# Performance work log

Measured on AMD Instinct MI355X. Metric: run time of the kernel, lower is better.

## Reference

```python
import jax, jax.numpy as jnp
import numpy as np

ALPHA = 0.4  # LeakyReLU negative slope used by the GAT


def _gat_head(h, W, a):
    # h: [N, F], W: [F, Fp], a: [2*Fp]; adjacency is all-ones so no masking
    Wh = h @ W                                   # [N, Fp]
    Fp = W.shape[1]
    e = jax.nn.leaky_relu(Wh @ a[:Fp][:, None] + (Wh @ a[Fp:])[None, :], ALPHA)
    att = jax.nn.softmax(e, axis=-1)             # [N, N]
    return att @ Wh                              # [N, Fp]


def _gat(h, W_heads, a_heads, W_gout, a_gout):
    # multi-head GAT: concat elu(head outputs), then single output attention layer
    heads = jax.vmap(_gat_head, in_axes=(None, 0, 0))(h, W_heads, a_heads)  # [H, N, Fp]
    x = jax.nn.elu(heads).transpose(1, 0, 2).reshape(h.shape[0], -1)        # [N, H*Fp]
    return jax.nn.elu(_gat_head(x, W_gout, a_gout))                          # [N, Cg]


def setup_inputs() -> dict:
    key = jax.random.key(0)
    ks = jax.random.split(key, 20)
    bs, R, S = 4, 512, 54
    h, w = 100, 152
    fc_dim, convs_dim4 = 1024, 512
    Cg, H, So = 256, 4, 128
    Fp = Cg // H
    sc = lambda k, shp, s=0.05: jax.random.normal(k, shp, dtype=jnp.float32) * s
    return {
        'region_f': jax.random.normal(ks[0], (bs * R, fc_dim), dtype=jnp.float32),
        'stuff_f': jax.random.normal(ks[1], (bs, convs_dim4, h, w), dtype=jnp.float32),
        'semseg_score': jax.random.normal(ks[2], (bs, S, h, w), dtype=jnp.float32),
        'W_rin': sc(ks[3], (fc_dim, Cg)), 'b_rin': jnp.zeros((Cg,), jnp.float32),
        'W_sin': sc(ks[4], (convs_dim4, Cg)), 'b_sin': jnp.zeros((Cg,), jnp.float32),
        'W_heads': sc(ks[5], (H, Cg, Fp), 0.1), 'a_heads': sc(ks[6], (H, 2 * Fp), 0.1),
        'W_gout': sc(ks[7], (H * Fp, Cg), 0.1), 'a_gout': sc(ks[8], (2 * Cg,), 0.1),
        'W_rout': sc(ks[9], (Cg, Cg)), 'b_rout': jnp.zeros((Cg,), jnp.float32),
        'W_sout': sc(ks[10], (Cg, So)), 'b_sout': jnp.zeros((So,), jnp.float32),
        'W_seg': sc(ks[11], (convs_dim4 + So, S)), 'b_seg': jnp.zeros((S,), jnp.float32),
    }


def reference(region_f, stuff_f, semseg_score,
              W_rin, b_rin, W_sin, b_sin,
              W_heads, a_heads, W_gout, a_gout,
              W_rout, b_rout, W_sout, b_sout,
              W_seg, b_seg):
    bs, Cd, h, w = stuff_f.shape
    S = semseg_score.shape[1]
    R = region_f.shape[0] // bs
    Cg = W_rin.shape[1]

    # node construction
    region_nodes = region_f @ W_rin + b_rin                           # [bs*R, Cg]
    score_flat = semseg_score.reshape(bs, S, h * w)
    class_center = jnp.einsum('bsn,bcn->bsc',
                              jax.nn.softmax(score_flat, axis=-1),
                              stuff_f.reshape(bs, Cd, h * w))          # [bs, S, Cd]
    class_nodes = class_center @ W_sin + b_sin                         # [bs, S, Cg]

    # per-image dense GAT over region + stuff nodes (batched via vmap)
    nodes = jnp.concatenate([region_nodes.reshape(bs, R, Cg), class_nodes], axis=1)
    graph_nodes = jax.vmap(lambda x: _gat(x, W_heads, a_heads, W_gout, a_gout))(nodes)
    new_region, new_class = graph_nodes[:, :R], graph_nodes[:, R:]

    # new box features: concat of original region features and projected graph features
    new_region_f = jnp.concatenate(
        [region_f, new_region.reshape(bs * R, Cg) @ W_rout + b_rout], axis=-1)

    # new stuff features: scatter class nodes back to pixels via class softmax
    new_class_nodes = new_class @ W_sout + b_sout                      # [bs, S, So]
    attn = jax.nn.softmax(score_flat, axis=1)                          # softmax over classes
    new_stuff = jnp.einsum('bsn,bso->bon', attn, new_class_nodes)      # [bs, So, h*w]
    new_stuff = new_stuff.reshape(bs, -1, h, w)

    # 1x1 conv seg head + x4 bilinear upsample (align_corners=False)
    seg_in = jnp.concatenate([stuff_f, new_stuff], axis=1)
    seg = jnp.einsum('bchw,co->bohw', seg_in, W_seg) + b_seg[None, :, None, None]
    segments = jax.image.resize(seg, (bs, S, 4 * h, 4 * w), method='bilinear')
    return new_region_f, segments
```

## Files before the change

kernel.cpp:

```cpp
#include <hip/hip_runtime.h>

#define HW 15200
#define SSD 54
#define NBATCH 4
#define NNODE 566
#define NPAD 576
#define CGD 256
#define CDD 512
#define NSPLIT 25
#define KSPAN 608

typedef __attribute__((ext_vector_type(4))) float f32x4;
typedef __attribute__((ext_vector_type(8))) short bf16x8;
typedef unsigned short ushort_t;

#define BT_RIN   0
#define BT_SIN   262144
#define BT_HEADS 393216
#define BT_GOUT  458752
#define BT_ROUT  524288
#define BT_SOUT  589824
#define BT_SEG2  622592
#define BT_TOTAL 630784

static constexpr long OFF_P     = 0;
static constexpr long OFF_CC    = OFF_P     + (long)NBATCH*SSD*HW;
static constexpr long OFF_NODES = OFF_CC    + (long)NBATCH*SSD*CDD;
static constexpr long OFF_WH    = OFF_NODES + (long)NBATCH*NNODE*CGD;
static constexpr long OFF_S1    = OFF_WH    + (long)16*NNODE*64;
static constexpr long OFF_S2    = OFF_S1    + 16*NPAD;
static constexpr long OFF_X     = OFF_S2    + 16*NPAD;
static constexpr long OFF_WH2   = OFF_X     + (long)NBATCH*NNODE*CGD;
static constexpr long OFF_S1B   = OFF_WH2   + (long)NBATCH*NNODE*CGD;
static constexpr long OFF_S2B   = OFF_S1B   + NBATCH*NPAD;
static constexpr long OFF_G     = OFF_S2B   + NBATCH*NPAD;
static constexpr long OFF_NCN   = OFF_G     + (long)NBATCH*NNODE*CGD;
static constexpr long OFF_SUMS  = OFF_NCN   + (long)NBATCH*SSD*128;
static constexpr long OFF_BT    = OFF_SUMS  + 256;
static constexpr long OFF_ASEG  = OFF_BT    + (BT_TOTAL/2 + 8);
static constexpr long OFF_SEG   = OFF_ASEG  + (long)NBATCH*64*576/2;
static constexpr long OFF_RFB   = OFF_SEG   + (long)NBATCH*SSD*HW;
static constexpr long OFF_WCOMB = OFF_RFB   + 1048576;
static constexpr long OFF_B2    = OFF_WCOMB + 8192;
static constexpr long OFF_ATTNB = OFF_B2    + 64;

__device__ inline float lrelu04(float x){ return x >= 0.f ? x : 0.4f*x; }
__device__ inline float eluf(float x){ return x > 0.f ? x : __expf(x) - 1.f; }
__device__ inline ushort_t f2bf(float f){
    unsigned u = __float_as_uint(f);
    return (ushort_t)((u + 0x7FFFu + ((u >> 16) & 1u)) >> 16);
}
__device__ inline float bf2f(ushort_t u){ return __uint_as_float((unsigned)u << 16); }
__device__ inline bf16x8 pack8(float4 lo, float4 hi){
    union { bf16x8 v; ushort_t u[8]; } p;
    p.u[0]=f2bf(lo.x); p.u[1]=f2bf(lo.y); p.u[2]=f2bf(lo.z); p.u[3]=f2bf(lo.w);
    p.u[4]=f2bf(hi.x); p.u[5]=f2bf(hi.y); p.u[6]=f2bf(hi.z); p.u[7]=f2bf(hi.w);
    return p.v;
}

__global__ __launch_bounds__(512)
void prep_softmax(const float* __restrict__ score, ushort_t* __restrict__ pb,
                  float* __restrict__ sums, ushort_t* __restrict__ attnb,
                  const float* __restrict__ rf, float* __restrict__ out_region,
                  ushort_t* __restrict__ rfb,
                  const float* __restrict__ W_seg, ushort_t* __restrict__ asegb,
                  const float* __restrict__ W_rin, const float* __restrict__ W_sin,
                  const float* __restrict__ W_heads, const float* __restrict__ W_gout,
                  const float* __restrict__ W_rout, const float* __restrict__ W_sout,
                  const float* __restrict__ b_sout,
                  ushort_t* __restrict__ bt, ushort_t* __restrict__ wcomb,
                  float* __restrict__ bias2, float* __restrict__ s1s2b_zero)
{
    int blk = blockIdx.x;
    int t = threadIdx.x;
    if (blk < 256) {
        int b = blk >> 6, s = blk & 63;
        ushort_t* prow = pb + ((long)b*64 + s)*HW;
        if (s >= SSD) {
            for (int i = t; i < HW; i += 512) prow[i] = 0;
            if (t == 0) sums[b*64 + s] = 1.f;
            return;
        }
        const float* row = score + ((long)b*SSD + s)*HW;
        __shared__ float red[8];
        float s_ = 0.f;
        for (int i = t; i < HW; i += 512) {
            float e = __expf(row[i]);
            s_ += e;
            prow[i] = f2bf(e);
        }
        #pragma unroll
        for (int off = 32; off >= 1; off >>= 1) s_ += __shfl_down(s_, off);
        if ((t & 63) == 0) red[t >> 6] = s_;
        __syncthreads();
        if (t == 0) {
            float tot = 0.f;
            #pragma unroll
            for (int u = 0; u < 8; ++u) tot += red[u];
            sums[b*64 + s] = tot;
        }
        return;
    }
    if (blk < 375) {
        long i = (long)(blk - 256)*512 + t;
        if (i >= (long)NBATCH*HW) return;
        int b = (int)(i / HW), n = (int)(i % HW);
        const float* sp = score + (long)b*SSD*HW + n;
        float v[SSD];
        float m = -1e30f;
        #pragma unroll
        for (int s = 0; s < SSD; ++s) { v[s] = sp[(long)s*HW]; m = fmaxf(m, v[s]); }
        float sum = 0.f;
        #pragma unroll
        for (int s = 0; s < SSD; ++s) { v[s] = __expf(v[s] - m); sum += v[s]; }
        float inv = 1.f / sum;
        ushort_t* ap = attnb + (long)b*64*HW + n;
        #pragma unroll
        for (int s = 0; s < SSD; ++s) ap[(long)s*HW] = f2bf(v[s] * inv);
        #pragma unroll
        for (int s = SSD; s < 64; ++s) ap[(long)s*HW] = 0;
        return;
    }
    long gid = (long)(blk - 375) * 512 + t;
    if (gid < 524288) {
        long row = gid / 256, col = gid % 256;
        float4 v = reinterpret_cast<const float4*>(rf)[gid];
        reinterpret_cast<float4*>(out_region)[row*320 + col] = v;
        union { ushort_t u[4]; uint2 q; } pk;
        pk.u[0]=f2bf(v.x); pk.u[1]=f2bf(v.y); pk.u[2]=f2bf(v.z); pk.u[3]=f2bf(v.w);
        reinterpret_cast<uint2*>(rfb)[gid] = pk.q;
        return;
    }
    gid -= 524288;
    if (gid < 131072) {
        int b = (int)(gid >> 15);
        int r = (int)(gid & 32767);
        int o = r >> 9, k = r & 511;
        asegb[(long)b*36864 + (long)o*576 + k] = f2bf(o < SSD ? W_seg[k*SSD + o] : 0.f);
        return;
    }
    gid -= 131072;
    if (gid < BT_TOTAL) {
        int i = (int)gid;
        float v;
        if (i < BT_SIN)        { int j=i;            int n=j>>10, k=j&1023; v = W_rin[k*256+n]; }
        else if (i < BT_HEADS) { int j=i-BT_SIN;     int n=j>>9,  k=j&511;  v = W_sin[k*256+n]; }
        else if (i < BT_GOUT)  { int j=i-BT_HEADS;   int h=j>>14, r=j&16383; int f=r>>8, k=r&255;
                                 v = W_heads[(h*256+k)*64+f]; }
        else if (i < BT_ROUT)  { int j=i-BT_GOUT;    int n=j>>8,  k=j&255;  v = W_gout[k*256+n]; }
        else if (i < BT_SOUT)  { int j=i-BT_ROUT;    int n=j>>8,  k=j&255;  v = W_rout[k*256+n]; }
        else if (i < BT_SEG2)  { int j=i-BT_SOUT;    int n=j>>8,  k=j&255;  v = W_sout[k*128+n]; }
        else                   { int j=i-BT_SEG2;    int o=j>>7,  k=j&127;
                                 v = (o < SSD) ? W_seg[(512+k)*SSD + o] : 0.f; }
        bt[i] = f2bf(v);
        return;
    }
    gid -= BT_TOTAL;
    if (gid < 16384) {
        int od = (int)(gid >> 8), k = (int)(gid & 255);
        float v = 0.f;
        if (od < SSD)
            for (int o = 0; o < 128; ++o)
                v += W_sout[k*128 + o] * W_seg[(512+o)*SSD + od];
        wcomb[(long)od*256 + k] = f2bf(v);
        return;
    }
    gid -= 16384;
    if (gid < 64) {
        int od = (int)gid;
        float v = 0.f;
        if (od < SSD)
            for (int o = 0; o < 128; ++o)
                v += b_sout[o] * W_seg[(512+o)*SSD + od];
        bias2[od] = v;
        return;
    }
    gid -= 64;
    if (gid < 2L*NBATCH*NPAD)
        s1s2b_zero[gid] = 0.f;
}

__global__ __launch_bounds__(256)
void cc_mfma_v3(const ushort_t* __restrict__ pb, const float* __restrict__ stuff,
                ushort_t* __restrict__ sbout, float* __restrict__ part)
{
    int bid = blockIdx.x;
    int g = (bid >> 6) * 8 + (bid & 7);
    if (g >= NSPLIT*NBATCH) return;
    int nt = (bid >> 3) & 7;
    int ks = g >> 2, b = g & 3;

    int w = threadIdx.x >> 6, l = threadIdx.x & 63;
    int lr = l & 15, lk = l >> 4;
    int n0 = nt*64 + w*16;
    const ushort_t* Prow = pb + ((long)b*64 + lr)*HW;
    const float*    Srow = stuff + ((long)b*CDD + n0 + lr)*HW;
    ushort_t*       Sout = sbout + ((long)b*CDD + n0 + lr)*HW;
    f32x4 acc[4] = {};
    int kbeg = ks * KSPAN;
    for (int k0 = kbeg; k0 < kbeg + KSPAN; k0 += 32) {
        int kk = k0 + lk*8;
        float4 lo = *(const float4*)&Srow[kk];
        float4 hi = *(const float4*)&Srow[kk + 4];
        bf16x8 bfv = pack8(lo, hi);
        *(bf16x8*)&Sout[kk] = bfv;
        #pragma unroll
        for (int mi = 0; mi < 4; ++mi) {
            bf16x8 af = *(const bf16x8*)&Prow[(long)mi*16*HW + kk];
            acc[mi] = __builtin_amdgcn_mfma_f32_16x16x32_bf16(af, bfv, acc[mi], 0, 0, 0);
        }
    }
    int c = n0 + lr;
    #pragma unroll
    for (int mi = 0; mi < 4; ++mi)
        #pragma unroll
        for (int r = 0; r < 4; ++r) {
            int m = mi*16 + lk*4 + r;
            part[(((long)b*NSPLIT + ks)*64 + m)*CDD + c] = acc[mi][r];
        }
}

__global__ __launch_bounds__(256)
void cc_reduce_kernel(const float* __restrict__ part, const float* __restrict__ sums,
                      float* __restrict__ cc)
{
    long i = (long)blockIdx.x * 256 + threadIdx.x;
    const long TOT = (long)NBATCH * SSD * CDD;
    if (i >= TOT) return;
    int b = (int)(i / (SSD * CDD));
    int rem = (int)(i % (SSD * CDD));
    int s = rem / CDD, c = rem % CDD;
    float acc = 0.f;
    for (int ks = 0; ks < NSPLIT; ++ks)
        acc += part[(((long)b*NSPLIT + ks)*64 + s)*CDD + c];
    cc[i] = acc * (1.f / sums[b*64 + s]);
}

template<bool AF32, int OUTMODE>
__device__ __forceinline__
void mm_body(int bx, int by, int bz,
             const void* __restrict__ Ap, const ushort_t* __restrict__ Bt,
             void* __restrict__ Cp, const float* __restrict__ bias,
             int M, int N, int K, int lda, int ldc,
             long sA, int zdivA, long sB, int zmodB, long sC)
{
    int z = bz;
    int w = threadIdx.x >> 6, l = threadIdx.x & 63;
    int lr = l & 15, lk = l >> 4;
    int m0 = bx * 64 + w * 16;
    int n0 = by * 64;
    const ushort_t* bt = Bt + (long)(z % zmodB) * sB;
    int mload = min(m0 + lr, M - 1);
    const float*    Af = (const float*)Ap    + (long)(z / zdivA) * sA + (long)mload * lda;
    const ushort_t* Ab = (const ushort_t*)Ap + (long)(z / zdivA) * sA + (long)mload * lda;
    f32x4 acc[4] = {};

    #pragma unroll 2
    for (int k0 = 0; k0 < K; k0 += 32) {
        int kk = k0 + lk * 8;
        bf16x8 af;
        if (AF32) {
            float4 lo = *(const float4*)&Af[kk];
            float4 hi = *(const float4*)&Af[kk + 4];
            af = pack8(lo, hi);
        } else {
            af = *(const bf16x8*)&Ab[kk];
        }
        #pragma unroll
        for (int j = 0; j < 4; ++j) {
            bf16x8 bf = *(const bf16x8*)&bt[(long)(n0 + j*16 + lr) * K + kk];
            acc[j] = __builtin_amdgcn_mfma_f32_16x16x32_bf16(af, bf, acc[j], 0, 0, 0);
        }
    }

    #pragma unroll
    for (int j = 0; j < 4; ++j) {
        int n = n0 + j*16 + lr;
        float bb = bias ? bias[n] : 0.f;
        #pragma unroll
        for (int r = 0; r < 4; ++r) {
            int m = m0 + lk*4 + r;
            if (OUTMODE == 2) {
                float v = acc[j][r] + bb;
                ((ushort_t*)Cp)[(long)z * sC + (long)n * ldc + m] =
                    (m < M) ? f2bf(v) : (ushort_t)0;
            } else {
                if (m >= M) continue;
                float v = acc[j][r] + bb;
                if (OUTMODE == 0)
                    ((float*)Cp)[(long)z * sC + (long)m * ldc + n] = v;
                else
                    ((ushort_t*)Cp)[(long)z * sC + (long)m * ldc + n] = f2bf(v);
            }
        }
    }
}

__global__ __launch_bounds__(256)
void nodes_both(const ushort_t* __restrict__ rfb, const ushort_t* __restrict__ btRin,
                const float* __restrict__ cc, const ushort_t* __restrict__ btSin,
                ushort_t* __restrict__ nodes,
                const float* __restrict__ b_rin, const float* __restrict__ b_sin)
{
    if (blockIdx.x < 8)
        mm_body<false, 1>(blockIdx.x, blockIdx.y, blockIdx.z,
                          rfb, btRin, nodes, b_rin,
                          512, 256, 1024, 1024, 256, 512L*1024, 1, 0, 1, (long)NNODE*CGD);
    else
        mm_body<true, 1>(0, blockIdx.y, blockIdx.z,
                         cc, btSin, nodes + 512L*CGD, b_sin,
                         SSD, 256, 512, 512, 256, (long)SSD*CDD, 1, 0, 1, (long)NNODE*CGD);
}

__global__ __launch_bounds__(256)
void wht_heads(const ushort_t* __restrict__ nodes, const ushort_t* __restrict__ btHeads,
               ushort_t* __restrict__ wht, const float* __restrict__ a_heads,
               float* __restrict__ s1, float* __restrict__ s2)
{
    int bx = blockIdx.x, z = blockIdx.y;
    int w = threadIdx.x >> 6, l = threadIdx.x & 63;
    int lr = l & 15, lk = l >> 4;
    int m0 = bx*64 + w*16;
    const ushort_t* bt = btHeads + (long)(z & 3) * (64L*256);
    int mload = min(m0 + lr, NNODE - 1);
    const ushort_t* Ab = nodes + (long)(z >> 2)*((long)NNODE*CGD) + (long)mload*CGD;
    f32x4 acc[4] = {};

    #pragma unroll 2
    for (int k0 = 0; k0 < 256; k0 += 32) {
        int kk = k0 + lk*8;
        bf16x8 af = *(const bf16x8*)&Ab[kk];
        #pragma unroll
        for (int j = 0; j < 4; ++j) {
            bf16x8 bf = *(const bf16x8*)&bt[(long)(j*16 + lr)*256 + kk];
            acc[j] = __builtin_amdgcn_mfma_f32_16x16x32_bf16(af, bf, acc[j], 0, 0, 0);
        }
    }

    const float* av = a_heads + (long)(z & 3)*128;
    ushort_t* Wout = wht + (long)z*(64L*NPAD);
    float p1[4] = {0.f,0.f,0.f,0.f}, p2[4] = {0.f,0.f,0.f,0.f};
    #pragma unroll
    for (int j = 0; j < 4; ++j) {
        int f = j*16 + lr;
        float c1 = av[f], c2 = av[64 + f];
        #pragma unroll
        for (int r = 0; r < 4; ++r) {
            int m = m0 + lk*4 + r;
            float v = acc[j][r];
            Wout[(long)f*NPAD + m] = (m < NNODE) ? f2bf(v) : (ushort_t)0;
            if (m < NNODE) { p1[r] += v*c1; p2[r] += v*c2; }
        }
    }
    #pragma unroll
    for (int r = 0; r < 4; ++r)
        #pragma unroll
        for (int off = 1; off < 16; off <<= 1) {
            p1[r] += __shfl_xor(p1[r], off);
            p2[r] += __shfl_xor(p2[r], off);
        }
    if (lr == 0) {
        #pragma unroll
        for (int r = 0; r < 4; ++r) {
            int m = m0 + lk*4 + r;
            if (m < NNODE) {
                s1[(long)z*NPAD + m] = p1[r];
                s2[(long)z*NPAD + m] = p2[r];
            }
        }
    }
}

__global__ __launch_bounds__(256)
void wht2_gout(const ushort_t* __restrict__ xbuf, const ushort_t* __restrict__ btGout,
               ushort_t* __restrict__ wht2, const float* __restrict__ a_gout,
               float* __restrict__ s1b, float* __restrict__ s2b)
{
    int bx = blockIdx.x, by = blockIdx.y, z = blockIdx.z;
    int w = threadIdx.x >> 6, l = threadIdx.x & 63;
    int lr = l & 15, lk = l >> 4;
    int m0 = bx*64 + w*16;
    int n0 = by*64;
    int mload = min(m0 + lr, NNODE - 1);
    const ushort_t* Ab = xbuf + (long)z*((long)NNODE*CGD) + (long)mload*CGD;
    f32x4 acc[4] = {};

    #pragma unroll 2
    for (int k0 = 0; k0 < 256; k0 += 32) {
        int kk = k0 + lk*8;
        bf16x8 af = *(const bf16x8*)&Ab[kk];
        #pragma unroll
        for (int j = 0; j < 4; ++j) {
            bf16x8 bf = *(const bf16x8*)&btGout[(long)(n0 + j*16 + lr)*256 + kk];
            acc[j] = __builtin_amdgcn_mfma_f32_16x16x32_bf16(af, bf, acc[j], 0, 0, 0);
        }
    }

    ushort_t* Wout = wht2 + (long)z*(256L*NPAD);
    float p1[4] = {0.f,0.f,0.f,0.f}, p2[4] = {0.f,0.f,0.f,0.f};
    #pragma unroll
    for (int j = 0; j < 4; ++j) {
        int f = n0 + j*16 + lr;
        float c1 = a_gout[f], c2 = a_gout[256 + f];
        #pragma unroll
        for (int r = 0; r < 4; ++r) {
            int m = m0 + lk*4 + r;
            float v = acc[j][r];
            Wout[(long)f*NPAD + m] = (m < NNODE) ? f2bf(v) : (ushort_t)0;
            if (m < NNODE) { p1[r] += v*c1; p2[r] += v*c2; }
        }
    }
    #pragma unroll
    for (int r = 0; r < 4; ++r)
        #pragma unroll
        for (int off = 1; off < 16; off <<= 1) {
            p1[r] += __shfl_xor(p1[r], off);
            p2[r] += __shfl_xor(p2[r], off);
        }
    if (lr == 0) {
        #pragma unroll
        for (int r = 0; r < 4; ++r) {
            int m = m0 + lk*4 + r;
            if (m < NNODE) {
                atomicAdd(&s1b[(long)z*NPAD + m], p1[r]);
                atomicAdd(&s2b[(long)z*NPAD + m], p2[r]);
            }
        }
    }
}

template<int F, int HEADMODE>
__global__ __launch_bounds__(256)
void att_mfma(const ushort_t* __restrict__ WhTall, const float* __restrict__ s1v,
              const float* __restrict__ s2v, ushort_t* __restrict__ outbuf)
{
    constexpr int FT = F / 16;
    int z = blockIdx.y;
    const ushort_t* W  = WhTall + (long)z * F * NPAD;
    const float* s1 = s1v + (long)z * NPAD;
    const float* s2 = s2v + (long)z * NPAD;
    int w = threadIdx.x >> 6, l = threadIdx.x & 63;
    int lr = l & 15, lk = l >> 4;

    __shared__ float s2sh[NPAD];
    __shared__ float redm[4];
    float mxl = -1e30f;
    for (int i = threadIdx.x; i < NPAD; i += 256) {
        float v = (i < NNODE) ? s2[i] : -1e30f;
        s2sh[i] = v;
        mxl = fmaxf(mxl, v);
    }
    #pragma unroll
    for (int off = 32; off >= 1; off >>= 1) mxl = fmaxf(mxl, __shfl_down(mxl, off));
    if (l == 0) redm[w] = mxl;
    __syncthreads();
    float s2max = fmaxf(fmaxf(redm[0], redm[1]), fmaxf(redm[2], redm[3]));

    int m0 = blockIdx.x * 64 + w * 16;
    float s1r = s1[min(m0 + lr, NNODE - 1)];
    float mrow = lrelu04(s1r + s2max);

    union { bf16x8 v; ushort_t u[8]; } onesu;
    #pragma unroll
    for (int u = 0; u < 8; ++u) onesu.u[u] = 0x3F80;
    bf16x8 ones = onesu.v;

    f32x4 acc[FT] = {};
    f32x4 accw = {};

    for (int j0 = 0; j0 < NPAD; j0 += 32) {
        float wv[8];
        #pragma unroll
        for (int u = 0; u < 8; ++u) {
            float e = lrelu04(s1r + s2sh[j0 + lk*8 + u]);
            wv[u] = __expf(e - mrow);
        }
        float4 lo = {wv[0], wv[1], wv[2], wv[3]};
        float4 hi = {wv[4], wv[5], wv[6], wv[7]};
        bf16x8 af = pack8(lo, hi);
        accw = __builtin_amdgcn_mfma_f32_16x16x32_bf16(af, ones, accw, 0, 0, 0);
        #pragma unroll
        for (int ft = 0; ft < FT; ++ft) {
            bf16x8 bf = *(const bf16x8*)&W[(long)(ft*16 + lr)*NPAD + j0 + lk*8];
            acc[ft] = __builtin_amdgcn_mfma_f32_16x16x32_bf16(af, bf, acc[ft], 0, 0, 0);
        }
    }

    #pragma unroll
    for (int r = 0; r < 4; ++r) {
        int m = m0 + lk*4 + r;
        if (m >= NNODE) continue;
        float inv = 1.f / accw[r];
        #pragma unroll
        for (int ft = 0; ft < FT; ++ft) {
            int f = ft*16 + lr;
            float v = eluf(acc[ft][r] * inv);
            if (HEADMODE) {
                int b = z >> 2, h = z & 3;
                outbuf[((long)(b*NNODE + m))*CGD + h*64 + f] = f2bf(v);
            } else {
                outbuf[((long)(z*NNODE + m))*CGD + f] = f2bf(v);
            }
        }
    }
}

__global__ __launch_bounds__(256)
void att_gout_m2(const ushort_t* __restrict__ wht2, const float* __restrict__ s1v,
                 const float* __restrict__ s2v, ushort_t* __restrict__ g,
                 const ushort_t* __restrict__ wcomb, const float* __restrict__ bias2,
                 ushort_t* __restrict__ asegm2)
{
    int bx = blockIdx.x, z = blockIdx.y;
    const ushort_t* W  = wht2 + (long)z * (256L*NPAD);
    const float* s1 = s1v + (long)z * NPAD;
    const float* s2 = s2v + (long)z * NPAD;
    int t = threadIdx.x;
    int w = t >> 6, l = t & 63;
    int lr = l & 15, lk = l >> 4;

    __shared__ float s2sh[NPAD];
    __shared__ float redm[4];
    __shared__ ushort_t gld[64][264];

    float mxl = -1e30f;
    for (int i = t; i < NPAD; i += 256) {
        float v = (i < NNODE) ? s2[i] : -1e30f;
        s2sh[i] = v;
        mxl = fmaxf(mxl, v);
    }
    if (bx == 8)
        for (int i = t; i < 10*264; i += 256) gld[54 + i/264][i%264] = 0;
    #pragma unroll
    for (int off = 32; off >= 1; off >>= 1) mxl = fmaxf(mxl, __shfl_down(mxl, off));
    if (l == 0) redm[w] = mxl;
    __syncthreads();
    float s2max = fmaxf(fmaxf(redm[0], redm[1]), fmaxf(redm[2], redm[3]));

    int m0 = bx * 64 + w * 16;
    float s1r = s1[min(m0 + lr, NNODE - 1)];
    float mrow = lrelu04(s1r + s2max);

    union { bf16x8 v; ushort_t u[8]; } onesu;
    #pragma unroll
    for (int u = 0; u < 8; ++u) onesu.u[u] = 0x3F80;
    bf16x8 ones = onesu.v;

    f32x4 acc[16] = {};
    f32x4 accw = {};

    for (int j0 = 0; j0 < NPAD; j0 += 32) {
        float wv[8];
        #pragma unroll
        for (int u = 0; u < 8; ++u) {
            float e = lrelu04(s1r + s2sh[j0 + lk*8 + u]);
            wv[u] = __expf(e - mrow);
        }
        float4 lo = {wv[0], wv[1], wv[2], wv[3]};
        float4 hi = {wv[4], wv[5], wv[6], wv[7]};
        bf16x8 af = pack8(lo, hi);
        accw = __builtin_amdgcn_mfma_f32_16x16x32_bf16(af, ones, accw, 0, 0, 0);
        #pragma unroll
        for (int ft = 0; ft < 16; ++ft) {
            bf16x8 bf = *(const bf16x8*)&W[(long)(ft*16 + lr)*NPAD + j0 + lk*8];
            acc[ft] = __builtin_amdgcn_mfma_f32_16x16x32_bf16(af, bf, acc[ft], 0, 0, 0);
        }
    }

    #pragma unroll
    for (int r = 0; r < 4; ++r) {
        int m = m0 + lk*4 + r;
        if (m >= NNODE) continue;
        float inv = 1.f / accw[r];
        #pragma unroll
        for (int ft = 0; ft < 16; ++ft) {
            int f = ft*16 + lr;
            ushort_t vb = f2bf(eluf(acc[ft][r] * inv));
            g[((long)(z*NNODE + m))*CGD + f] = vb;
            if (bx == 8) gld[m - 512][f] = vb;
        }
    }

    if (bx == 8) {
        __syncthreads();
        f32x4 acc2[4] = {};
        #pragma unroll 2
        for (int k0 = 0; k0 < 256; k0 += 32) {
            int kk = k0 + lk*8;
            bf16x8 af = *(const bf16x8*)&gld[w*16 + lr][kk];
            #pragma unroll
            for (int j = 0; j < 4; ++j) {
                bf16x8 bf = *(const bf16x8*)&wcomb[(long)(j*16 + lr)*256 + kk];
                acc2[j] = __builtin_amdgcn_mfma_f32_16x16x32_bf16(af, bf, acc2[j], 0, 0, 0);
            }
        }
        #pragma unroll
        for (int j = 0; j < 4; ++j) {
            int n = j*16 + lr;
            float bb = bias2[n];
            #pragma unroll
            for (int r = 0; r < 4; ++r) {
                int m = w*16 + lk*4 + r;
                asegm2[(long)z*36864 + (long)n*576 + m] =
                    (m < SSD) ? f2bf(acc2[j][r] + bb) : (ushort_t)0;
            }
        }
    }
}

__device__ __forceinline__
void seg_body(int nt, int b,
              const ushort_t* __restrict__ stuffb, const ushort_t* __restrict__ attnb,
              const ushort_t* __restrict__ asegb, const float* __restrict__ b_seg,
              float* __restrict__ seg)
{
    int w = threadIdx.x >> 6, l = threadIdx.x & 63;
    int lr = l & 15, lk = l >> 4;
    int n0 = nt*128 + w*32;
    const ushort_t* A = asegb + (long)b*36864;
    const ushort_t* S = stuffb + (long)b*CDD*HW;
    const ushort_t* T = attnb + (long)b*64*HW;
    f32x4 acc[4][2] = {};
    int n1 = min(n0 + lr, HW-1);
    int n2 = min(n0 + 16 + lr, HW-1);

    for (int k0 = 0; k0 < 576; k0 += 32) {
        const ushort_t* Bsrc = (k0 < 512) ? S + (long)k0*HW : T + (long)(k0-512)*HW;
        long kb = (long)(lk*8)*HW;
        union { bf16x8 v; ushort_t u[8]; } b0, b1;
        #pragma unroll
        for (int u = 0; u < 8; ++u) {
            b0.u[u] = Bsrc[kb + (long)u*HW + n1];
            b1.u[u] = Bsrc[kb + (long)u*HW + n2];
        }
        #pragma unroll
        for (int ot = 0; ot < 4; ++ot) {
            bf16x8 af = *(const bf16x8*)&A[(ot*16 + lr)*576 + k0 + lk*8];
            acc[ot][0] = __builtin_amdgcn_mfma_f32_16x16x32_bf16(af, b0.v, acc[ot][0], 0,0,0);
            acc[ot][1] = __builtin_amdgcn_mfma_f32_16x16x32_bf16(af, b1.v, acc[ot][1], 0,0,0);
        }
    }

    #pragma unroll
    for (int ot = 0; ot < 4; ++ot) {
        #pragma unroll
        for (int r = 0; r < 4; ++r) {
            int o = ot*16 + lk*4 + r;
            if (o >= SSD) continue;
            float bb = b_seg[o];
            int na = n0 + lr, nb = n0 + 16 + lr;
            if (na < HW) seg[((long)b*SSD + o)*HW + na] = acc[ot][0][r] + bb;
            if (nb < HW) seg[((long)b*SSD + o)*HW + nb] = acc[ot][1][r] + bb;
        }
    }
}

__global__ __launch_bounds__(256)
void rout_seg(const ushort_t* __restrict__ g_bf, const ushort_t* __restrict__ btRout,
              float* __restrict__ outreg, const float* __restrict__ b_rout,
              const ushort_t* __restrict__ stuffb, const ushort_t* __restrict__ attnb,
              const ushort_t* __restrict__ asegb, const float* __restrict__ b_seg,
              float* __restrict__ segb)
{
    int bid = blockIdx.x;
    if (bid < 128) {
        int x = bid & 7, y = (bid >> 3) & 3, z = bid >> 5;
        mm_body<false, 0>(x, y, z, g_bf, btRout, outreg, b_rout,
                          512, 256, 256, 256, 1280, (long)NNODE*CGD, 1, 0, 1, 512L*1280);
    } else {
        int sid = bid - 128;
        seg_body(sid % 119, sid / 119, stuffb, attnb, asegb, b_seg, segb);
    }
}

__global__ __launch_bounds__(256)
void resize_v2_kernel(const float* __restrict__ seg, float* __restrict__ out)
{
    long u = (long)blockIdx.x * 256 + threadIdx.x;
    const long TOT4 = (long)NBATCH * SSD * 400 * 152;
    if (u >= TOT4) return;
    int m = (int)(u % 152);
    long r = u / 152;
    int y = (int)(r % 400);
    long c = r / 400;
    float fy = y * 0.25f - 0.375f;
    int y0 = (int)floorf(fy);
    float wy = fy - (float)y0;
    int y0c = max(y0, 0), y1c = min(y0 + 1, 99);
    const float* sp = seg + c * HW;
    int xm = max(m - 1, 0), xp = min(m + 1, 151);
    float r0a = sp[y0c * 152 + xm], r0b = sp[y0c * 152 + m], r0c = sp[y0c * 152 + xp];
    float r1a = sp[y1c * 152 + xm], r1b = sp[y1c * 152 + m], r1c = sp[y1c * 152 + xp];
    float ra = r0a + wy * (r1a - r0a);
    float rb = r0b + wy * (r1b - r0b);
    float rc = r0c + wy * (r1c - r0c);
    float4 o4;
    o4.x = 0.375f * ra + 0.625f * rb;
    o4.y = 0.125f * ra + 0.875f * rb;
    o4.z = 0.875f * rb + 0.125f * rc;
    o4.w = 0.625f * rb + 0.375f * rc;
    reinterpret_cast<float4*>(out)[u] = o4;
}

extern "C" void kernel_launch(void* const* d_in, const int* in_sizes, int n_in,
                              void* d_out, int out_size, void* d_ws, size_t ws_size,
                              hipStream_t stream)
{
    const float* region_f = (const float*)d_in[0];
    const float* stuff    = (const float*)d_in[1];
    const float* score    = (const float*)d_in[2];
    const float* W_rin    = (const float*)d_in[3];
    const float* b_rin    = (const float*)d_in[4];
    const float* W_sin    = (const float*)d_in[5];
    const float* b_sin    = (const float*)d_in[6];
    const float* W_heads  = (const float*)d_in[7];
    const float* a_heads  = (const float*)d_in[8];
    const float* W_gout   = (const float*)d_in[9];
    const float* a_gout   = (const float*)d_in[10];
    const float* W_rout   = (const float*)d_in[11];
    const float* b_rout   = (const float*)d_in[12];
    const float* W_sout   = (const float*)d_in[13];
    const float* b_sout   = (const float*)d_in[14];
    const float* W_seg    = (const float*)d_in[15];
    const float* b_seg    = (const float*)d_in[16];

    float* out = (float*)d_out;
    float* ws  = (float*)d_ws;

    ushort_t* pb   = (ushort_t*)(ws + OFF_P);
    float* cc      = ws + OFF_CC;
    ushort_t* nodes_bf = (ushort_t*)(ws + OFF_NODES);
    ushort_t* wht  = (ushort_t*)(ws + OFF_WH);
    float* s1      = ws + OFF_S1;
    float* s2      = ws + OFF_S2;
    ushort_t* xbuf_bf = (ushort_t*)(ws + OFF_X);
    ushort_t* wht2 = (ushort_t*)(ws + OFF_WH2);
    float* s1b     = ws + OFF_S1B;
    float* s2b     = ws + OFF_S2B;
    ushort_t* g_bf = (ushort_t*)(ws + OFF_G);
    float* sums    = ws + OFF_SUMS;
    ushort_t* bt   = (ushort_t*)(ws + OFF_BT);
    ushort_t* asegb = (ushort_t*)(ws + OFF_ASEG);
    float* segb    = ws + OFF_SEG;
    float* cc_p    = ws + OFF_SEG;
    ushort_t* rfb  = (ushort_t*)(ws + OFF_RFB);
    ushort_t* wcomb = (ushort_t*)(ws + OFF_WCOMB);
    float* bias2v  = ws + OFF_B2;
    ushort_t* attnb = (ushort_t*)(ws + OFF_ATTNB);

    float* out_region = out;
    float* out_seg    = out + 2048L*1280;
    ushort_t* stuffb  = (ushort_t*)out_seg;

    prep_softmax<<<2929, 512, 0, stream>>>(score, pb, sums, attnb,
                                           region_f, out_region, rfb, W_seg, asegb,
                                           W_rin, W_sin, W_heads, W_gout, W_rout, W_sout,
                                           b_sout, bt, wcomb, bias2v, s1b);

    cc_mfma_v3<<<832, 256, 0, stream>>>(pb, stuff, stuffb, cc_p);
    cc_reduce_kernel<<<(NBATCH*SSD*CDD + 255)/256, 256, 0, stream>>>(cc_p, sums, cc);

    nodes_both<<<dim3(9, 4, 4), 256, 0, stream>>>(
        rfb, bt + BT_RIN, cc, bt + BT_SIN, nodes_bf, b_rin, b_sin);

    wht_heads<<<dim3(9, 16), 256, 0, stream>>>(
        nodes_bf, bt + BT_HEADS, wht, a_heads, s1, s2);

    att_mfma<64, 1><<<dim3(9, 16), 256, 0, stream>>>(wht, s1, s2, xbuf_bf);

    wht2_gout<<<dim3(9, 4, 4), 256, 0, stream>>>(
        xbuf_bf, bt + BT_GOUT, wht2, a_gout, s1b, s2b);

    att_gout_m2<<<dim3(9, 4), 256, 0, stream>>>(
        wht2, s1b, s2b, g_bf, wcomb, bias2v, asegb + 512);

    rout_seg<<<604, 256, 0, stream>>>(
        g_bf, bt + BT_ROUT, out_region + 1024, b_rout,
        stuffb, attnb, asegb, b_seg, segb);

    resize_v2_kernel<<<((long)NBATCH*SSD*400*152 + 255)/256, 256, 0, stream>>>(segb, out_seg);
}
```

Baseline: 323.6 us.

## Replace split-K partial buffer and reduce kernel with atomics, merge prep into cc kernel

The class-context split-K GEMM now accumulates its partial sums straight into a zeroed buffer with atomicAdd, which removes the partial-sum buffer and the separate reduction kernel. The softmax normalisation by row sums moves into the nodes kernel's A-operand load. Prep work that does not depend on the softmax sums (class softmax, region copy, weight packing) is folded into the same launch as the cc GEMM so the two overlap, and the first kernel now only does the row exps and zeroing. In exchange, fp32 atomic contention is added and summation order becomes nondeterministic.

```diff
diff --git a/kernel.cpp b/kernel.cpp
--- a/kernel.cpp
+++ b/kernel.cpp
@@ -25,7 +25,7 @@
 
 static constexpr long OFF_P     = 0;
 static constexpr long OFF_CC    = OFF_P     + (long)NBATCH*SSD*HW;
-static constexpr long OFF_NODES = OFF_CC    + (long)NBATCH*SSD*CDD;
+static constexpr long OFF_NODES = OFF_CC    + (long)NBATCH*64*CDD;
 static constexpr long OFF_WH    = OFF_NODES + (long)NBATCH*NNODE*CGD;
 static constexpr long OFF_S1    = OFF_WH    + (long)16*NNODE*64;
 static constexpr long OFF_S2    = OFF_S1    + 16*NPAD;
@@ -34,8 +34,7 @@
 static constexpr long OFF_S1B   = OFF_WH2   + (long)NBATCH*NNODE*CGD;
 static constexpr long OFF_S2B   = OFF_S1B   + NBATCH*NPAD;
 static constexpr long OFF_G     = OFF_S2B   + NBATCH*NPAD;
-static constexpr long OFF_NCN   = OFF_G     + (long)NBATCH*NNODE*CGD;
-static constexpr long OFF_SUMS  = OFF_NCN   + (long)NBATCH*SSD*128;
+static constexpr long OFF_SUMS  = OFF_G     + (long)NBATCH*NNODE*CGD;
 static constexpr long OFF_BT    = OFF_SUMS  + 256;
 static constexpr long OFF_ASEG  = OFF_BT    + (BT_TOTAL/2 + 8);
 static constexpr long OFF_SEG   = OFF_ASEG  + (long)NBATCH*64*576/2;
@@ -59,17 +58,9 @@
 }
 
 __global__ __launch_bounds__(512)
-void prep_softmax(const float* __restrict__ score, ushort_t* __restrict__ pb,
-                  float* __restrict__ sums, ushort_t* __restrict__ attnb,
-                  const float* __restrict__ rf, float* __restrict__ out_region,
-                  ushort_t* __restrict__ rfb,
-                  const float* __restrict__ W_seg, ushort_t* __restrict__ asegb,
-                  const float* __restrict__ W_rin, const float* __restrict__ W_sin,
-                  const float* __restrict__ W_heads, const float* __restrict__ W_gout,
-                  const float* __restrict__ W_rout, const float* __restrict__ W_sout,
-                  const float* __restrict__ b_sout,
-                  ushort_t* __restrict__ bt, ushort_t* __restrict__ wcomb,
-                  float* __restrict__ bias2, float* __restrict__ s1s2b_zero)
+void softmax_p(const float* __restrict__ score, ushort_t* __restrict__ pb,
+               float* __restrict__ sums, float* __restrict__ s1s2b_zero,
+               float* __restrict__ ccp)
 {
     int blk = blockIdx.x;
     int t = threadIdx.x;
@@ -101,10 +92,66 @@
         }
         return;
     }
-    if (blk < 375) {
-        long i = (long)(blk - 256)*512 + t;
-        if (i >= (long)NBATCH*HW) return;
-        int b = (int)(i / HW), n = (int)(i % HW);
+    long gid = (long)(blk - 256)*512 + t;
+    if (gid < 4608) { s1s2b_zero[gid] = 0.f; return; }
+    gid -= 4608;
+    if (gid < (long)NBATCH*64*CDD) ccp[gid] = 0.f;
+}
+
+__global__ __launch_bounds__(256)
+void cc_prep(const ushort_t* __restrict__ pb, const float* __restrict__ stuff,
+             ushort_t* __restrict__ sbout, float* __restrict__ ccp,
+             const float* __restrict__ score, ushort_t* __restrict__ attnb,
+             const float* __restrict__ rf, float* __restrict__ out_region,
+             ushort_t* __restrict__ rfb,
+             const float* __restrict__ W_seg, ushort_t* __restrict__ asegb,
+             const float* __restrict__ W_rin, const float* __restrict__ W_sin,
+             const float* __restrict__ W_heads, const float* __restrict__ W_gout,
+             const float* __restrict__ W_rout, const float* __restrict__ W_sout,
+             const float* __restrict__ b_sout,
+             ushort_t* __restrict__ bt, ushort_t* __restrict__ wcomb,
+             float* __restrict__ bias2)
+{
+    int bid = blockIdx.x;
+    if (bid < 832) {
+        int g = (bid >> 6) * 8 + (bid & 7);
+        if (g >= NSPLIT*NBATCH) return;
+        int nt = (bid >> 3) & 7;
+        int ks = g >> 2, b = g & 3;
+
+        int w = threadIdx.x >> 6, l = threadIdx.x & 63;
+        int lr = l & 15, lk = l >> 4;
+        int n0 = nt*64 + w*16;
+        const ushort_t* Prow = pb + ((long)b*64 + lr)*HW;
+        const float*    Srow = stuff + ((long)b*CDD + n0 + lr)*HW;
+        ushort_t*       Sout = sbout + ((long)b*CDD + n0 + lr)*HW;
+        f32x4 acc[4] = {};
+        int kbeg = ks * KSPAN;
+        for (int k0 = kbeg; k0 < kbeg + KSPAN; k0 += 32) {
+            int kk = k0 + lk*8;
+            float4 lo = *(const float4*)&Srow[kk];
+            float4 hi = *(const float4*)&Srow[kk + 4];
+            bf16x8 bfv = pack8(lo, hi);
+            *(bf16x8*)&Sout[kk] = bfv;
+            #pragma unroll
+            for (int mi = 0; mi < 4; ++mi) {
+                bf16x8 af = *(const bf16x8*)&Prow[(long)mi*16*HW + kk];
+                acc[mi] = __builtin_amdgcn_mfma_f32_16x16x32_bf16(af, bfv, acc[mi], 0, 0, 0);
+            }
+        }
+        int c = n0 + lr;
+        #pragma unroll
+        for (int mi = 0; mi < 4; ++mi)
+            #pragma unroll
+            for (int r = 0; r < 4; ++r) {
+                int m = mi*16 + lk*4 + r;
+                atomicAdd(&ccp[((long)b*64 + m)*CDD + c], acc[mi][r]);
+            }
+        return;
+    }
+    long gid = (long)(bid - 832) * 256 + threadIdx.x;
+    if (gid < (long)NBATCH*HW) {
+        int b = (int)(gid / HW), n = (int)(gid % HW);
         const float* sp = score + (long)b*SSD*HW + n;
         float v[SSD];
         float m = -1e30f;
@@ -121,7 +168,7 @@
         for (int s = SSD; s < 64; ++s) ap[(long)s*HW] = 0;
         return;
     }
-    long gid = (long)(blk - 375) * 512 + t;
+    gid -= (long)NBATCH*HW;
     if (gid < 524288) {
         long row = gid / 256, col = gid % 256;
         float4 v = reinterpret_cast<const float4*>(rf)[gid];
@@ -173,67 +220,7 @@
             for (int o = 0; o < 128; ++o)
                 v += b_sout[o] * W_seg[(512+o)*SSD + od];
         bias2[od] = v;
-        return;
-    }
-    gid -= 64;
-    if (gid < 2L*NBATCH*NPAD)
-        s1s2b_zero[gid] = 0.f;
-}
-
-__global__ __launch_bounds__(256)
-void cc_mfma_v3(const ushort_t* __restrict__ pb, const float* __restrict__ stuff,
-                ushort_t* __restrict__ sbout, float* __restrict__ part)
-{
-    int bid = blockIdx.x;
-    int g = (bid >> 6) * 8 + (bid & 7);
-    if (g >= NSPLIT*NBATCH) return;
-    int nt = (bid >> 3) & 7;
-    int ks = g >> 2, b = g & 3;
-
-    int w = threadIdx.x >> 6, l = threadIdx.x & 63;
-    int lr = l & 15, lk = l >> 4;
-    int n0 = nt*64 + w*16;
-    const ushort_t* Prow = pb + ((long)b*64 + lr)*HW;
-    const float*    Srow = stuff + ((long)b*CDD + n0 + lr)*HW;
-    ushort_t*       Sout = sbout + ((long)b*CDD + n0 + lr)*HW;
-    f32x4 acc[4] = {};
-    int kbeg = ks * KSPAN;
-    for (int k0 = kbeg; k0 < kbeg + KSPAN; k0 += 32) {
-        int kk = k0 + lk*8;
-        float4 lo = *(const float4*)&Srow[kk];
-        float4 hi = *(const float4*)&Srow[kk + 4];
-        bf16x8 bfv = pack8(lo, hi);
-        *(bf16x8*)&Sout[kk] = bfv;
-        #pragma unroll
-        for (int mi = 0; mi < 4; ++mi) {
-            bf16x8 af = *(const bf16x8*)&Prow[(long)mi*16*HW + kk];
-            acc[mi] = __builtin_amdgcn_mfma_f32_16x16x32_bf16(af, bfv, acc[mi], 0, 0, 0);
-        }
-    }
-    int c = n0 + lr;
-    #pragma unroll
-    for (int mi = 0; mi < 4; ++mi)
-        #pragma unroll
-        for (int r = 0; r < 4; ++r) {
-            int m = mi*16 + lk*4 + r;
-            part[(((long)b*NSPLIT + ks)*64 + m)*CDD + c] = acc[mi][r];
-        }
-}
-
-__global__ __launch_bounds__(256)
-void cc_reduce_kernel(const float* __restrict__ part, const float* __restrict__ sums,
-                      float* __restrict__ cc)
-{
-    long i = (long)blockIdx.x * 256 + threadIdx.x;
-    const long TOT = (long)NBATCH * SSD * CDD;
-    if (i >= TOT) return;
-    int b = (int)(i / (SSD * CDD));
-    int rem = (int)(i % (SSD * CDD));
-    int s = rem / CDD, c = rem % CDD;
-    float acc = 0.f;
-    for (int ks = 0; ks < NSPLIT; ++ks)
-        acc += part[(((long)b*NSPLIT + ks)*64 + s)*CDD + c];
-    cc[i] = acc * (1.f / sums[b*64 + s]);
+    }
 }
 
 template<bool AF32, int OUTMODE>
@@ -298,18 +285,51 @@
 
 __global__ __launch_bounds__(256)
 void nodes_both(const ushort_t* __restrict__ rfb, const ushort_t* __restrict__ btRin,
-                const float* __restrict__ cc, const ushort_t* __restrict__ btSin,
-                ushort_t* __restrict__ nodes,
+                const float* __restrict__ ccp, const float* __restrict__ sums,
+                const ushort_t* __restrict__ btSin, ushort_t* __restrict__ nodes,
                 const float* __restrict__ b_rin, const float* __restrict__ b_sin)
 {
-    if (blockIdx.x < 8)
+    if (blockIdx.x < 8) {
         mm_body<false, 1>(blockIdx.x, blockIdx.y, blockIdx.z,
                           rfb, btRin, nodes, b_rin,
                           512, 256, 1024, 1024, 256, 512L*1024, 1, 0, 1, (long)NNODE*CGD);
-    else
-        mm_body<true, 1>(0, blockIdx.y, blockIdx.z,
-                         cc, btSin, nodes + 512L*CGD, b_sin,
-                         SSD, 256, 512, 512, 256, (long)SSD*CDD, 1, 0, 1, (long)NNODE*CGD);
+        return;
+    }
+    int by = blockIdx.y, bz = blockIdx.z;
+    int w = threadIdx.x >> 6, l = threadIdx.x & 63;
+    int lr = l & 15, lk = l >> 4;
+    int m0 = w * 16, n0 = by * 64;
+    int mload = min(m0 + lr, SSD - 1);
+    const float* Af = ccp + ((long)bz*64 + mload)*CDD;
+    float inv = 1.f / sums[bz*64 + mload];
+    f32x4 acc[4] = {};
+
+    #pragma unroll 2
+    for (int k0 = 0; k0 < CDD; k0 += 32) {
+        int kk = k0 + lk * 8;
+        float4 lo = *(const float4*)&Af[kk];
+        float4 hi = *(const float4*)&Af[kk + 4];
+        lo.x *= inv; lo.y *= inv; lo.z *= inv; lo.w *= inv;
+        hi.x *= inv; hi.y *= inv; hi.z *= inv; hi.w *= inv;
+        bf16x8 af = pack8(lo, hi);
+        #pragma unroll
+        for (int j = 0; j < 4; ++j) {
+            bf16x8 bf = *(const bf16x8*)&btSin[(long)(n0 + j*16 + lr) * CDD + kk];
+            acc[j] = __builtin_amdgcn_mfma_f32_16x16x32_bf16(af, bf, acc[j], 0, 0, 0);
+        }
+    }
+
+    #pragma unroll
+    for (int j = 0; j < 4; ++j) {
+        int n = n0 + j*16 + lr;
+        float bb = b_sin[n];
+        #pragma unroll
+        for (int r = 0; r < 4; ++r) {
+            int m = m0 + lk*4 + r;
+            if (m >= SSD) continue;
+            nodes[(long)bz*NNODE*CGD + (long)(512 + m)*CGD + n] = f2bf(acc[j][r] + bb);
+        }
+    }
 }
 
 __global__ __launch_bounds__(256)
@@ -728,7 +748,7 @@
     float* ws  = (float*)d_ws;
 
     ushort_t* pb   = (ushort_t*)(ws + OFF_P);
-    float* cc      = ws + OFF_CC;
+    float* ccp     = ws + OFF_CC;
     ushort_t* nodes_bf = (ushort_t*)(ws + OFF_NODES);
     ushort_t* wht  = (ushort_t*)(ws + OFF_WH);
     float* s1      = ws + OFF_S1;
@@ -742,7 +762,6 @@
     ushort_t* bt   = (ushort_t*)(ws + OFF_BT);
     ushort_t* asegb = (ushort_t*)(ws + OFF_ASEG);
     float* segb    = ws + OFF_SEG;
-    float* cc_p    = ws + OFF_SEG;
     ushort_t* rfb  = (ushort_t*)(ws + OFF_RFB);
     ushort_t* wcomb = (ushort_t*)(ws + OFF_WCOMB);
     float* bias2v  = ws + OFF_B2;
@@ -752,16 +771,15 @@
     float* out_seg    = out + 2048L*1280;
     ushort_t* stuffb  = (ushort_t*)out_seg;
 
-    prep_softmax<<<2929, 512, 0, stream>>>(score, pb, sums, attnb,
-                                           region_f, out_region, rfb, W_seg, asegb,
-                                           W_rin, W_sin, W_heads, W_gout, W_rout, W_sout,
-                                           b_sout, bt, wcomb, bias2v, s1b);
-
-    cc_mfma_v3<<<832, 256, 0, stream>>>(pb, stuff, stuffb, cc_p);
-    cc_reduce_kernel<<<(NBATCH*SSD*CDD + 255)/256, 256, 0, stream>>>(cc_p, sums, cc);
+    softmax_p<<<521, 512, 0, stream>>>(score, pb, sums, s1b, ccp);
+
+    cc_prep<<<6158, 256, 0, stream>>>(pb, stuff, stuffb, ccp, score, attnb,
+                                      region_f, out_region, rfb, W_seg, asegb,
+                                      W_rin, W_sin, W_heads, W_gout, W_rout, W_sout,
+                                      b_sout, bt, wcomb, bias2v);
 
     nodes_both<<<dim3(9, 4, 4), 256, 0, stream>>>(
-        rfb, bt + BT_RIN, cc, bt + BT_SIN, nodes_bf, b_rin, b_sin);
+        rfb, bt + BT_RIN, ccp, sums, bt + BT_SIN, nodes_bf, b_rin, b_sin);
 
     wht_heads<<<dim3(9, 16), 256, 0, stream>>>(
         nodes_bf, bt + BT_HEADS, wht, a_heads, s1, s2);
```

Measured after the change: 315.8 us. 1.02x faster.
